# Performance work log

Measured on AMD Instinct MI355X. Metric: run time of the kernel, lower is better.

The kernel has to match this reference:

```python
import jax, jax.numpy as jnp
import numpy as np

B, P, F, H, C = 128, 2048, 512, 256, 16

def setup_inputs() -> dict:
    key = jax.random.key(0)
    ks = jax.random.split(key, 8)
    s_in = 1.0 / np.sqrt(F)
    s_h = 1.0 / np.sqrt(H)
    s_p = 1.0 / np.sqrt(P + C)
    return {
        "x": jax.random.normal(ks[0], (B, P, F), jnp.float32),
        "adj": jax.random.uniform(ks[1], (P, P), jnp.float32) / P,  # row-scaled dense adjacency
        "clinical": jax.random.normal(ks[2], (B, C), jnp.float32),
        "W1": jax.random.normal(ks[3], (F, H), jnp.float32) * s_in,
        "b1": jnp.zeros((H,), jnp.float32),
        "W2": jax.random.normal(ks[4], (H, H), jnp.float32) * s_h,
        "b2": jnp.zeros((H,), jnp.float32),
        "lw1": jax.random.normal(ks[5], (H,), jnp.float32) * s_h,
        "lb1": jnp.zeros((1,), jnp.float32),
        "lw2": jax.random.normal(ks[6], (P + C,), jnp.float32) * s_p,
        "lb2": jnp.zeros((1,), jnp.float32),
    }

def gcn(x, adj, W, b):
    # GraphConvolution: adj @ (x @ W) + b, batched over leading dim
    support = jnp.einsum('bpf,fh->bph', x, W)
    return jnp.einsum('pq,bqh->bph', adj, support) + b

def reference(x, adj, clinical, W1, b1, W2, b2, lw1, lb1, lw2, lb2):
    h = jnp.tanh(gcn(x, adj, W1, b1))          # [B,P,H]; dropout is no-op in eval
    h = jnp.tanh(gcn(h, adj, W2, b2))          # [B,P,H]
    s = jnp.tanh(jnp.einsum('bph,h->bp', h, lw1) + lb1)  # lin1 + squeeze -> [B,P]
    z = jnp.concatenate([s, clinical], axis=1)  # [B,P+C]
    return z @ lw2[:, None] + lb2               # lin2 -> [B,1]
```

## Files before the change

### kernel.cpp

```cpp
#include <hip/hip_runtime.h>
#include <hip/hip_bf16.h>

#define B_ 128
#define P_ 2048
#define F_ 512
#define H_ 256
#define C_ 16

typedef __attribute__((ext_vector_type(8))) __bf16 bf16x8;
typedef __attribute__((ext_vector_type(4))) float f32x4;

__device__ __forceinline__ unsigned short f2bf(float f) {
  union { float f; unsigned u; } x; x.f = f;
  unsigned r = x.u + 0x7fffu + ((x.u >> 16) & 1u);
  return (unsigned short)(r >> 16);
}
__device__ __forceinline__ float bf2f(unsigned short u) {
  union { unsigned u; float f; } x; x.u = ((unsigned)u) << 16;
  return x.f;
}

typedef __attribute__((address_space(1))) void as1_void;
typedef __attribute__((address_space(3))) void as3_void;
__device__ __forceinline__ void gload_lds16(const void* g, void* l) {
  __builtin_amdgcn_global_load_lds((as1_void*)g, (as3_void*)l, 16, 0, 0);
}

template<int EPI, bool BF32>
__global__ __launch_bounds__(256) void gemm_nt(
    const unsigned short* __restrict__ A, long aStr,
    const void* __restrict__ Bt_, long bStr,
    unsigned short* __restrict__ C, long cStr,
    const float* __restrict__ bias,
    int M, int N, int K)
{
  __shared__ unsigned short As[128 * 64];
  __shared__ unsigned short Bs[128 * 64];

  const int zb = blockIdx.z;
  const unsigned short* Ab = A + (long)zb * aStr;
  unsigned short* Cb = C + (long)zb * cStr;
  const unsigned short* Btb = nullptr;
  const float* Btf = nullptr;
  if constexpr (BF32) Btf = (const float*)Bt_ + (long)zb * bStr;
  else                Btb = (const unsigned short*)Bt_ + (long)zb * bStr;

  const int tid  = threadIdx.x;
  const int lane = tid & 63;
  const int wave = tid >> 6;
  const int wr = wave >> 1, wc = wave & 1;
  const int l16 = lane & 15, lhi = lane >> 4;
  const int m0 = blockIdx.y * 128, n0 = blockIdx.x * 128;

  f32x4 acc[4][4] = {};

  for (int k0 = 0; k0 < K; k0 += 64) {
#pragma unroll
    for (int i = 0; i < 4; ++i) {
      int e = i * 2048 + tid * 8;
      gload_lds16(Ab + (long)(m0 + (e >> 6)) * K + k0 + (e & 63), As + e);
    }
    if constexpr (!BF32) {
#pragma unroll
      for (int i = 0; i < 4; ++i) {
        int e = i * 2048 + tid * 8;
        gload_lds16(Btb + (long)(n0 + (e >> 6)) * K + k0 + (e & 63), Bs + e);
      }
    } else {
#pragma unroll
      for (int i = 0; i < 8; ++i) {
        int e = i * 1024 + tid * 4;
        float4 v = *(const float4*)(Btf + (long)(n0 + (e >> 6)) * K + k0 + (e & 63));
        ushort4 o; o.x = f2bf(v.x); o.y = f2bf(v.y); o.z = f2bf(v.z); o.w = f2bf(v.w);
        *(ushort4*)(Bs + e) = o;
      }
    }
    __syncthreads();

#pragma unroll
    for (int kk = 0; kk < 64; kk += 32) {
      bf16x8 af[4], bfr[4];
#pragma unroll
      for (int m = 0; m < 4; ++m)
        af[m] = *(const bf16x8*)&As[(wr * 64 + m * 16 + l16) * 64 + kk + lhi * 8];
#pragma unroll
      for (int n = 0; n < 4; ++n)
        bfr[n] = *(const bf16x8*)&Bs[(wc * 64 + n * 16 + l16) * 64 + kk + lhi * 8];
#pragma unroll
      for (int m = 0; m < 4; ++m)
#pragma unroll
        for (int n = 0; n < 4; ++n)
          acc[m][n] = __builtin_amdgcn_mfma_f32_16x16x32_bf16(af[m], bfr[n], acc[m][n], 0, 0, 0);
    }
    __syncthreads();
  }

#pragma unroll
  for (int m = 0; m < 4; ++m) {
#pragma unroll
    for (int n = 0; n < 4; ++n) {
      int col = n0 + wc * 64 + n * 16 + l16;
      float bv = 0.f;
      if constexpr (EPI == 1) bv = bias[col];
#pragma unroll
      for (int j = 0; j < 4; ++j) {
        int row = m0 + wr * 64 + m * 16 + lhi * 4 + j;
        float v = acc[m][n][j];
        if constexpr (EPI == 1) v = tanhf(v + bv);
        Cb[(long)row * N + col] = f2bf(v);
      }
    }
  }
}

__global__ __launch_bounds__(256) void cvt_bf16(const float* __restrict__ in,
                                                unsigned short* __restrict__ out, int n4) {
  int i = blockIdx.x * 256 + threadIdx.x;
  if (i >= n4) return;
  float4 v = ((const float4*)in)[i];
  ushort4 o; o.x = f2bf(v.x); o.y = f2bf(v.y); o.z = f2bf(v.z); o.w = f2bf(v.w);
  ((ushort4*)out)[i] = o;
}

__global__ __launch_bounds__(256) void tcvt_bf16(const float* __restrict__ in,
                                                 unsigned short* __restrict__ out, int R, int Cc) {
  int idx = blockIdx.x * 256 + threadIdx.x;
  if (idx >= R * Cc) return;
  int r = idx / Cc, c = idx - r * Cc;
  out[c * R + r] = f2bf(in[idx]);
}

__global__ __launch_bounds__(256) void rowdot_tanh(const unsigned short* __restrict__ h2,
    const float* __restrict__ lw1, const float* __restrict__ lb1, float* __restrict__ s) {
  int row  = blockIdx.x * 4 + (threadIdx.x >> 6);
  int lane = threadIdx.x & 63;
  ushort4 v = ((const ushort4*)(h2 + (long)row * H_))[lane];
  float4  w = ((const float4*)lw1)[lane];
  float sum = bf2f(v.x) * w.x + bf2f(v.y) * w.y + bf2f(v.z) * w.z + bf2f(v.w) * w.w;
#pragma unroll
  for (int off = 32; off > 0; off >>= 1) sum += __shfl_xor(sum, off, 64);
  if (lane == 0) s[row] = tanhf(sum + lb1[0]);
}

__global__ __launch_bounds__(256) void final_dot(const float* __restrict__ s,
    const float* __restrict__ clin, const float* __restrict__ lw2,
    const float* __restrict__ lb2, float* __restrict__ out) {
  int b = blockIdx.x, t = threadIdx.x;
  float sum = 0.f;
#pragma unroll
  for (int i = 0; i < P_ / 256; ++i) { int p = i * 256 + t; sum += s[b * P_ + p] * lw2[p]; }
  if (t < C_) sum += clin[b * C_ + t] * lw2[P_ + t];
#pragma unroll
  for (int off = 32; off > 0; off >>= 1) sum += __shfl_xor(sum, off, 64);
  __shared__ float red[4];
  if ((t & 63) == 0) red[t >> 6] = sum;
  __syncthreads();
  if (t == 0) out[b] = red[0] + red[1] + red[2] + red[3] + lb2[0];
}

extern "C" void kernel_launch(void* const* d_in, const int* in_sizes, int n_in,
                              void* d_out, int out_size, void* d_ws, size_t ws_size,
                              hipStream_t stream) {
  const float* x    = (const float*)d_in[0];
  const float* adj  = (const float*)d_in[1];
  const float* clin = (const float*)d_in[2];
  const float* W1   = (const float*)d_in[3];
  const float* b1   = (const float*)d_in[4];
  const float* W2   = (const float*)d_in[5];
  const float* b2   = (const float*)d_in[6];
  const float* lw1  = (const float*)d_in[7];
  const float* lb1  = (const float*)d_in[8];
  const float* lw2  = (const float*)d_in[9];
  const float* lb2  = (const float*)d_in[10];
  float* out = (float*)d_out;

  char* w = (char*)d_ws;
  unsigned short* adjb = (unsigned short*)(w);
  unsigned short* W1t  = (unsigned short*)(w + 8388608);
  unsigned short* W2t  = (unsigned short*)(w + 8650752);
  float*          sbuf = (float*)(w + 8781824);
  unsigned short* bufA = (unsigned short*)(w + 9830400);
  unsigned short* bufB = (unsigned short*)(w + 144048128);

  hipLaunchKernelGGL(cvt_bf16, dim3(P_ * P_ / 4 / 256), dim3(256), 0, stream,
                     adj, adjb, P_ * P_ / 4);
  hipLaunchKernelGGL(tcvt_bf16, dim3((F_ * H_ + 255) / 256), dim3(256), 0, stream,
                     W1, W1t, F_, H_);
  hipLaunchKernelGGL(tcvt_bf16, dim3((H_ * H_ + 255) / 256), dim3(256), 0, stream,
                     W2, W2t, H_, H_);

  hipLaunchKernelGGL((gemm_nt<0, true>), dim3(P_ / 128, H_ / 128, B_), dim3(256), 0, stream,
      W1t, 0L, (const void*)x, (long)P_ * F_, bufA, (long)H_ * P_,
      (const float*)nullptr, H_, P_, F_);

  hipLaunchKernelGGL((gemm_nt<1, false>), dim3(H_ / 128, P_ / 128, B_), dim3(256), 0, stream,
      adjb, 0L, (const void*)bufA, (long)H_ * P_, bufB, (long)P_ * H_,
      b1, P_, H_, P_);

  hipLaunchKernelGGL((gemm_nt<0, false>), dim3(P_ / 128, H_ / 128, B_), dim3(256), 0, stream,
      W2t, 0L, (const void*)bufB, (long)P_ * H_, bufA, (long)H_ * P_,
      (const float*)nullptr, H_, P_, H_);

  hipLaunchKernelGGL((gemm_nt<1, false>), dim3(H_ / 128, P_ / 128, B_), dim3(256), 0, stream,
      adjb, 0L, (const void*)bufA, (long)H_ * P_, bufB, (long)P_ * H_,
      b2, P_, H_, P_);

  hipLaunchKernelGGL(rowdot_tanh, dim3(B_ * P_ / 4), dim3(256), 0, stream,
                     bufB, lw1, lb1, sbuf);

  hipLaunchKernelGGL(final_dot, dim3(B_), dim3(256), 0, stream,
                     sbuf, clin, lw2, lb2, out);
}
```

Before: 1.712 ms.

## Fuse batched adjacency GEMMs into one large 256x256-tile pipelined GEMM

The two batched adj@support GEMMs become a single GEMM with N = B*H, so adj is multiplied against all batches at once in a P x (B*H) layout. A new 512-thread kernel with 256x256 tiles, an XOR-swizzled LDS layout, double-buffered direct-to-LDS loads interleaved with MFMA phases, a block swizzle and s_setprio is meant to raise reuse and MFMA utilisation. Downstream kernels get leading-dimension parameters so they can read the new [P][B][H] layout, and the bias index is masked to H. The cost is more complex synchronisation and higher register and LDS pressure.

```diff
diff --git a/kernel.cpp b/kernel.cpp
--- a/kernel.cpp
+++ b/kernel.cpp
@@ -26,11 +26,136 @@
   __builtin_amdgcn_global_load_lds((as1_void*)g, (as3_void*)l, 16, 0, 0);
 }
 
+__global__ __launch_bounds__(512, 2) void gemm256(
+    const unsigned short* __restrict__ A,
+    const unsigned short* __restrict__ Bt,
+    unsigned short* __restrict__ C,
+    const float* __restrict__ bias,
+    int M, int N, int K)
+{
+  __shared__ unsigned short lds[65536];
+
+  const int tid  = threadIdx.x;
+  const int lane = tid & 63;
+  const int wv   = tid >> 6;
+  const int wr   = wv >> 2, wc = wv & 3;
+  const int l16  = lane & 15, lhi = lane >> 4;
+  const int NT   = K >> 6;
+
+  {
+  }
+  const int nwg = gridDim.x, cpx = nwg >> 3;
+  const int swz = (blockIdx.x & 7) * cpx + (blockIdx.x >> 3);
+  const int ntm = M >> 8;
+  const int m0 = (swz % ntm) * 256;
+  const int n0 = (swz / ntm) * 256;
+
+  f32x4 acc[2][2][4][2] = {};
+
+  auto stage = [&](int op, int half, int t) {
+    const int ts = t < NT ? t : NT - 1;
+    const unsigned short* src = op ? Bt : A;
+    const int row0 = (op ? n0 : m0) + half * 128;
+    unsigned short* ldst = lds + ((t & 1) << 15) + (op << 14) + (half << 13) + tid * 8;
+    const int rsub = tid >> 3;
+    const int k16  = (tid & 7) ^ (rsub & 7);
+    const long kk  = (long)ts * 64 + k16 * 8;
+    gload_lds16(src + (long)(row0 + rsub) * K + kk, ldst);
+    gload_lds16(src + (long)(row0 + 64 + rsub) * K + kk, ldst + 4096);
+  };
+
+  stage(0, 0, 0); stage(0, 1, 0); stage(1, 0, 0); stage(1, 1, 0);
+  stage(1, 0, 1); stage(0, 1, 1);
+  asm volatile("s_waitcnt vmcnt(4)" ::: "memory");
+  __builtin_amdgcn_s_barrier();
+
+#pragma unroll 1
+  for (int t = 0; t < NT; ++t) {
+    bf16x8 a[2][4], b[2][2];
+    const int bufo = (t & 1) << 15;
+
+    auto loadA = [&](int mh) {
+#pragma unroll
+      for (int ks = 0; ks < 2; ++ks)
+#pragma unroll
+        for (int mf = 0; mf < 4; ++mf) {
+          int r = wr * 128 + mh * 64 + mf * 16 + l16;
+          int k16 = ks * 4 + lhi;
+          a[ks][mf] = *(const bf16x8*)&lds[bufo + (r << 6) + ((k16 ^ (r & 7)) << 3)];
+        }
+    };
+    auto loadB = [&](int nh) {
+#pragma unroll
+      for (int ks = 0; ks < 2; ++ks)
+#pragma unroll
+        for (int nf = 0; nf < 2; ++nf) {
+          int r = wc * 64 + nh * 32 + nf * 16 + l16;
+          int k16 = ks * 4 + lhi;
+          b[ks][nf] = *(const bf16x8*)&lds[bufo + 16384 + (r << 6) + ((k16 ^ (r & 7)) << 3)];
+        }
+    };
+    auto domfma = [&](int mh, int nh) {
+      __builtin_amdgcn_s_setprio(1);
+#pragma unroll
+      for (int ks = 0; ks < 2; ++ks)
+#pragma unroll
+        for (int mf = 0; mf < 4; ++mf)
+#pragma unroll
+          for (int nf = 0; nf < 2; ++nf)
+            acc[mh][nh][mf][nf] = __builtin_amdgcn_mfma_f32_16x16x32_bf16(
+                a[ks][mf], b[ks][nf], acc[mh][nh][mf][nf], 0, 0, 0);
+      __builtin_amdgcn_s_setprio(0);
+    };
+
+#define MIDSYNC  __builtin_amdgcn_s_barrier(); \
+                 asm volatile("s_waitcnt lgkmcnt(0)" ::: "memory"); \
+                 __builtin_amdgcn_sched_barrier(0);
+#define ENDSYNC  __builtin_amdgcn_s_barrier(); \
+                 asm volatile("" ::: "memory");
+
+    loadA(0); loadB(0);
+    stage(0, 0, t + 1);
+    MIDSYNC; domfma(0, 0); ENDSYNC;
+
+    loadA(1);
+    stage(1, 1, t + 1);
+    MIDSYNC; domfma(1, 0); ENDSYNC;
+
+    loadB(1);
+    stage(1, 0, t + 2);
+    MIDSYNC; domfma(1, 1); ENDSYNC;
+
+    loadA(0);
+    stage(0, 1, t + 2);
+    asm volatile("s_waitcnt vmcnt(4)" ::: "memory");
+    MIDSYNC; domfma(0, 1); ENDSYNC;
+  }
+#undef MIDSYNC
+#undef ENDSYNC
+
+#pragma unroll
+  for (int mh = 0; mh < 2; ++mh)
+#pragma unroll
+    for (int nh = 0; nh < 2; ++nh)
+#pragma unroll
+      for (int mf = 0; mf < 4; ++mf)
+#pragma unroll
+        for (int nf = 0; nf < 2; ++nf) {
+          int col = n0 + wc * 64 + nh * 32 + nf * 16 + l16;
+          float bv = bias[col & (H_ - 1)];
+#pragma unroll
+          for (int j = 0; j < 4; ++j) {
+            int row = m0 + wr * 128 + mh * 64 + mf * 16 + lhi * 4 + j;
+            C[(long)row * N + col] = f2bf(tanhf(acc[mh][nh][mf][nf][j] + bv));
+          }
+        }
+}
+
 template<int EPI, bool BF32>
 __global__ __launch_bounds__(256) void gemm_nt(
-    const unsigned short* __restrict__ A, long aStr,
-    const void* __restrict__ Bt_, long bStr,
-    unsigned short* __restrict__ C, long cStr,
+    const unsigned short* __restrict__ A, long aStr, int ldA,
+    const void* __restrict__ Bt_, long bStr, int ldB,
+    unsigned short* __restrict__ C, long cStr, int ldC,
     const float* __restrict__ bias,
     int M, int N, int K)
 {
@@ -58,19 +183,19 @@
 #pragma unroll
     for (int i = 0; i < 4; ++i) {
       int e = i * 2048 + tid * 8;
-      gload_lds16(Ab + (long)(m0 + (e >> 6)) * K + k0 + (e & 63), As + e);
+      gload_lds16(Ab + (long)(m0 + (e >> 6)) * ldA + k0 + (e & 63), As + e);
     }
     if constexpr (!BF32) {
 #pragma unroll
       for (int i = 0; i < 4; ++i) {
         int e = i * 2048 + tid * 8;
-        gload_lds16(Btb + (long)(n0 + (e >> 6)) * K + k0 + (e & 63), Bs + e);
+        gload_lds16(Btb + (long)(n0 + (e >> 6)) * ldB + k0 + (e & 63), Bs + e);
       }
     } else {
 #pragma unroll
       for (int i = 0; i < 8; ++i) {
         int e = i * 1024 + tid * 4;
-        float4 v = *(const float4*)(Btf + (long)(n0 + (e >> 6)) * K + k0 + (e & 63));
+        float4 v = *(const float4*)(Btf + (long)(n0 + (e >> 6)) * ldB + k0 + (e & 63));
         ushort4 o; o.x = f2bf(v.x); o.y = f2bf(v.y); o.z = f2bf(v.z); o.w = f2bf(v.w);
         *(ushort4*)(Bs + e) = o;
       }
@@ -101,13 +226,13 @@
     for (int n = 0; n < 4; ++n) {
       int col = n0 + wc * 64 + n * 16 + l16;
       float bv = 0.f;
-      if constexpr (EPI == 1) bv = bias[col];
+      if constexpr (EPI == 1) bv = bias[col & (H_ - 1)];
 #pragma unroll
       for (int j = 0; j < 4; ++j) {
         int row = m0 + wr * 64 + m * 16 + lhi * 4 + j;
         float v = acc[m][n][j];
         if constexpr (EPI == 1) v = tanhf(v + bv);
-        Cb[(long)row * N + col] = f2bf(v);
+        Cb[(long)row * ldC + col] = f2bf(v);
       }
     }
   }
@@ -130,16 +255,17 @@
   out[c * R + r] = f2bf(in[idx]);
 }
 
-__global__ __launch_bounds__(256) void rowdot_tanh(const unsigned short* __restrict__ h2,
+__global__ __launch_bounds__(256) void rowdot_tanh(const unsigned short* __restrict__ h2m,
     const float* __restrict__ lw1, const float* __restrict__ lb1, float* __restrict__ s) {
-  int row  = blockIdx.x * 4 + (threadIdx.x >> 6);
+  int i = blockIdx.x * 4 + (threadIdx.x >> 6);
   int lane = threadIdx.x & 63;
-  ushort4 v = ((const ushort4*)(h2 + (long)row * H_))[lane];
+  int p = i >> 7, b = i & 127;
+  ushort4 v = ((const ushort4*)(h2m + (long)p * (B_ * H_) + b * H_))[lane];
   float4  w = ((const float4*)lw1)[lane];
   float sum = bf2f(v.x) * w.x + bf2f(v.y) * w.y + bf2f(v.z) * w.z + bf2f(v.w) * w.w;
 #pragma unroll
   for (int off = 32; off > 0; off >>= 1) sum += __shfl_xor(sum, off, 64);
-  if (lane == 0) s[row] = tanhf(sum + lb1[0]);
+  if (lane == 0) s[b * P_ + p] = tanhf(sum + lb1[0]);
 }
 
 __global__ __launch_bounds__(256) void final_dot(const float* __restrict__ s,
@@ -190,20 +316,18 @@
                      W2, W2t, H_, H_);
 
   hipLaunchKernelGGL((gemm_nt<0, true>), dim3(P_ / 128, H_ / 128, B_), dim3(256), 0, stream,
-      W1t, 0L, (const void*)x, (long)P_ * F_, bufA, (long)H_ * P_,
+      W1t, 0L, F_, (const void*)x, (long)P_ * F_, F_, bufA, (long)H_ * P_, P_,
       (const float*)nullptr, H_, P_, F_);
 
-  hipLaunchKernelGGL((gemm_nt<1, false>), dim3(H_ / 128, P_ / 128, B_), dim3(256), 0, stream,
-      adjb, 0L, (const void*)bufA, (long)H_ * P_, bufB, (long)P_ * H_,
-      b1, P_, H_, P_);
+  hipLaunchKernelGGL(gemm256, dim3((P_ / 256) * (B_ * H_ / 256)), dim3(512), 0, stream,
+      adjb, bufA, bufB, b1, P_, B_ * H_, P_);
 
   hipLaunchKernelGGL((gemm_nt<0, false>), dim3(P_ / 128, H_ / 128, B_), dim3(256), 0, stream,
-      W2t, 0L, (const void*)bufB, (long)P_ * H_, bufA, (long)H_ * P_,
+      W2t, 0L, H_, (const void*)bufB, 256L, B_ * H_, bufA, (long)H_ * P_, P_,
       (const float*)nullptr, H_, P_, H_);
 
-  hipLaunchKernelGGL((gemm_nt<1, false>), dim3(H_ / 128, P_ / 128, B_), dim3(256), 0, stream,
-      adjb, 0L, (const void*)bufA, (long)H_ * P_, bufB, (long)P_ * H_,
-      b2, P_, H_, P_);
+  hipLaunchKernelGGL(gemm256, dim3((P_ / 256) * (B_ * H_ / 256)), dim3(512), 0, stream,
+      adjb, bufA, bufB, b2, P_, B_ * H_, P_);
 
   hipLaunchKernelGGL(rowdot_tanh, dim3(B_ * P_ / 4), dim3(256), 0, stream,
                      bufB, lw1, lb1, sbuf);
```

New measurement: 1.437 ms. 1.19x faster.
